# Kernel tuning notes

Hardware: AMD Instinct MI355X
Metric: run time of the kernel (lower is better)

## Reference

```python
import jax, jax.numpy as jnp
import numpy as np

N_NODES = 50000
N_EDGES = 600000
DIM = 128


def setup_inputs() -> dict:
    key = jax.random.key(0)
    k1, k2, k3 = jax.random.split(key, 3)
    x = jax.random.normal(k1, (N_NODES, DIM), dtype=jnp.float32)
    edge_index = jax.random.randint(k2, (2, N_EDGES), 0, N_NODES, dtype=jnp.int64)
    # Xavier-uniform linear weight, torch layout [out_dim, in_dim]
    limit = float(np.sqrt(6.0 / (DIM + DIM)))
    W = jax.random.uniform(k3, (DIM, DIM), dtype=jnp.float32, minval=-limit, maxval=limit)
    return {"x": x, "edge_index": edge_index, "N": N_NODES, "W": W}


def reference(x, edge_index, N, W):
    src, dst = edge_index[0], edge_index[1]
    # in-degree via scatter-add of ones
    deg = jnp.zeros((N,), dtype=x.dtype).at[dst].add(1.0)
    deg_inv_sqrt = jax.lax.rsqrt(deg + 1.0)  # (deg + 1)^-0.5
    h = x * deg_inv_sqrt[:, None]                      # [N, D]
    # gather source features, scatter-add into destinations
    agg = jnp.zeros((N, x.shape[-1]), dtype=x.dtype).at[dst].add(h[src])
    agg = (agg + x) * deg_inv_sqrt[:, None]
    # Linear (no bias, torch weight layout) + ReLU
    return jax.nn.relu(agg @ W.T)
```

## Files before the change

kernel.cpp:

```cpp
#include <hip/hip_runtime.h>

#define DIM 128
#define CAP 48

typedef __attribute__((ext_vector_type(8))) short short8;
typedef __attribute__((ext_vector_type(4))) float floatx4;

__device__ inline unsigned bf16pack2(float a, float b) {
    unsigned ua = __float_as_uint(a), ub = __float_as_uint(b);
    ua = (ua + 0x7fffu + ((ua >> 16) & 1u)) >> 16;
    ub = (ub + 0x7fffu + ((ub >> 16) & 1u)) >> 16;
    return ua | (ub << 16);
}
__device__ inline float bflo(unsigned u) { return __uint_as_float(u << 16); }
__device__ inline float bfhi(unsigned u) { return __uint_as_float(u & 0xffff0000u); }

__global__ __launch_bounds__(256) void prep_kernel(int* __restrict__ degi, int nclr4,
                                                   int clearBlocks,
                                                   const float4* __restrict__ W4,
                                                   uint4* __restrict__ wbf,
                                                   const int* __restrict__ ei, int E,
                                                   int* __restrict__ flag) {
    int b = blockIdx.x;
    if (b < clearBlocks) {
        int i = b * 256 + threadIdx.x;
        if (i < nclr4) ((uint4*)degi)[i] = (uint4){0u, 0u, 0u, 0u};
    } else if (b < clearBlocks + 8) {
        int gw = (b - clearBlocks) * 256 + threadIdx.x;
        if (gw < 2048) {
            float4 lo = W4[(size_t)gw * 2];
            float4 hi = W4[(size_t)gw * 2 + 1];
            uint4 o;
            o.x = bf16pack2(lo.x, lo.y);
            o.y = bf16pack2(lo.z, lo.w);
            o.z = bf16pack2(hi.x, hi.y);
            o.w = bf16pack2(hi.z, hi.w);
            wbf[gw] = o;
        }
    } else {
        __shared__ int nz;
        if (threadIdx.x == 0) nz = 0;
        __syncthreads();
        int found = 0;
        for (int i = threadIdx.x; i < 2048; i += 256)
            if (i < E && ei[2 * i + 1] != 0) found = 1;
        if (found) atomicOr(&nz, 1);
        __syncthreads();
        if (threadIdx.x == 0) *flag = (nz == 0) ? 1 : 0;
    }
}

__global__ __launch_bounds__(256) void insert_kernel(const int* __restrict__ ei, int E,
                                                     unsigned M8,
                                                     const int* __restrict__ flag,
                                                     int* __restrict__ degi,
                                                     int* __restrict__ ssrc) {
    int is64 = *flag;
    unsigned cls = blockIdx.x & 7;
    int tstride4 = (gridDim.x >> 3) * 256 * 4;
    int t0 = ((blockIdx.x >> 3) * 256 + threadIdx.x) * 4;

    for (int e0 = t0; e0 < E; e0 += tstride4) {
        int s[4], d[4];
        if (is64) {
            const int* sw = ei + (size_t)2 * e0;
            int4 a0 = *(const int4*)sw;
            int4 a1 = *(const int4*)(sw + 4);
            s[0] = a0.x; s[1] = a0.z; s[2] = a1.x; s[3] = a1.z;
            const int* dw = ei + (size_t)2 * E + (size_t)2 * e0;
            int4 q0 = *(const int4*)dw;
            int4 q1 = *(const int4*)(dw + 4);
            d[0] = q0.x; d[1] = q0.z; d[2] = q1.x; d[3] = q1.z;
        } else {
            int4 a = *(const int4*)(ei + e0);
            s[0] = a.x; s[1] = a.y; s[2] = a.z; s[3] = a.w;
            int4 q = *(const int4*)(ei + (size_t)E + e0);
            d[0] = q.x; d[1] = q.y; d[2] = q.z; d[3] = q.w;
        }
#pragma unroll
        for (int k = 0; k < 4; ++k) {
            int e = e0 + k;
            if (e >= E) break;
            unsigned p = (unsigned)(((unsigned long long)(unsigned)d[k] * M8) >> 32);
            if (p != cls) continue;
            int slot = atomicAdd(&degi[d[k]], 1);
            if (slot < CAP)
                ssrc[(size_t)d[k] * CAP + slot] = s[k];
        }
    }
}

__global__ __launch_bounds__(256) void scale_kernel(const float4* __restrict__ x4,
                                                    const int* __restrict__ degi,
                                                    uint4* __restrict__ xh, int N) {
    int g = blockIdx.x * 256 + threadIdx.x;
    if (g >= N * 16) return;
    int n = g >> 4;
    float c = rsqrtf((float)degi[n] + 1.0f);
    float4 lo = x4[(size_t)g * 2];
    float4 hi = x4[(size_t)g * 2 + 1];
    uint4 o;
    o.x = bf16pack2(lo.x * c, lo.y * c);
    o.y = bf16pack2(lo.z * c, lo.w * c);
    o.z = bf16pack2(hi.x * c, hi.y * c);
    o.w = bf16pack2(hi.z * c, hi.w * c);
    xh[g] = o;
}

__global__ __launch_bounds__(256) void gather_kernel(const int* __restrict__ degi,
                                                     const int* __restrict__ ssrc,
                                                     const uint4* __restrict__ xh,
                                                     uint4* __restrict__ t, int N) {
    int g = threadIdx.x >> 4;
    int lane = threadIdx.x & 15;
    int n = blockIdx.x * 16 + g;
    if (n >= N) return;
    int deg = degi[n];
    int cnt = deg < CAP ? deg : CAP;
    const int* seg = ssrc + (size_t)n * CAP;

    uint4 self = xh[(size_t)n * 16 + lane];
    float acc[8] = {0.f, 0.f, 0.f, 0.f, 0.f, 0.f, 0.f, 0.f};

#define ADD8(v)                                            \
    {                                                      \
        acc[0] += bflo(v.x); acc[1] += bfhi(v.x);          \
        acc[2] += bflo(v.y); acc[3] += bfhi(v.y);          \
        acc[4] += bflo(v.z); acc[5] += bfhi(v.z);          \
        acc[6] += bflo(v.w); acc[7] += bfhi(v.w);          \
    }

    int j = 0;
    for (; j + 7 < cnt; j += 8) {
        int s0 = seg[j], s1 = seg[j + 1], s2 = seg[j + 2], s3 = seg[j + 3];
        int s4 = seg[j + 4], s5 = seg[j + 5], s6 = seg[j + 6], s7 = seg[j + 7];
        uint4 v0 = xh[(size_t)s0 * 16 + lane];
        uint4 v1 = xh[(size_t)s1 * 16 + lane];
        uint4 v2 = xh[(size_t)s2 * 16 + lane];
        uint4 v3 = xh[(size_t)s3 * 16 + lane];
        uint4 v4 = xh[(size_t)s4 * 16 + lane];
        uint4 v5 = xh[(size_t)s5 * 16 + lane];
        uint4 v6 = xh[(size_t)s6 * 16 + lane];
        uint4 v7 = xh[(size_t)s7 * 16 + lane];
        ADD8(v0); ADD8(v1); ADD8(v2); ADD8(v3);
        ADD8(v4); ADD8(v5); ADD8(v6); ADD8(v7);
    }
    if (j + 3 < cnt) {
        int s0 = seg[j], s1 = seg[j + 1], s2 = seg[j + 2], s3 = seg[j + 3];
        uint4 v0 = xh[(size_t)s0 * 16 + lane];
        uint4 v1 = xh[(size_t)s1 * 16 + lane];
        uint4 v2 = xh[(size_t)s2 * 16 + lane];
        uint4 v3 = xh[(size_t)s3 * 16 + lane];
        ADD8(v0); ADD8(v1); ADD8(v2); ADD8(v3);
        j += 4;
    }
    for (; j < cnt; ++j) {
        uint4 v = xh[(size_t)seg[j] * 16 + lane];
        ADD8(v);
    }
#undef ADD8

    float dn = rsqrtf((float)deg + 1.0f);
    uint4 o;
    o.x = bf16pack2(bflo(self.x) + acc[0] * dn, bfhi(self.x) + acc[1] * dn);
    o.y = bf16pack2(bflo(self.y) + acc[2] * dn, bfhi(self.y) + acc[3] * dn);
    o.z = bf16pack2(bflo(self.z) + acc[4] * dn, bfhi(self.z) + acc[5] * dn);
    o.w = bf16pack2(bflo(self.w) + acc[6] * dn, bfhi(self.w) + acc[7] * dn);
    t[(size_t)n * 16 + lane] = o;
}

__global__ __launch_bounds__(256) void gemm_relu_kernel(const char* __restrict__ t,
                                                        const char* __restrict__ wbf,
                                                        float* __restrict__ out, int N) {
    int tid = threadIdx.x;
    int w = tid >> 6, l = tid & 63;
    int q = l >> 4, m = l & 15;
    int wrow0 = blockIdx.x * 128 + w * 32;

    short8 a[2][4];
#pragma unroll
    for (int rf = 0; rf < 2; ++rf) {
        int r = wrow0 + rf * 16 + m;
        if (r > N - 1) r = N - 1;
        const char* rb = t + (size_t)r * 256 + q * 16;
#pragma unroll
        for (int c = 0; c < 4; ++c)
            a[rf][c] = *(const short8*)(rb + 64 * c);
    }

    floatx4 acc[2][8];
#pragma unroll
    for (int rf = 0; rf < 2; ++rf)
#pragma unroll
        for (int cf = 0; cf < 8; ++cf)
            acc[rf][cf] = (floatx4){0.f, 0.f, 0.f, 0.f};

#pragma unroll
    for (int c = 0; c < 4; ++c) {
#pragma unroll
        for (int cf = 0; cf < 8; ++cf) {
            short8 b = *(const short8*)(wbf + (size_t)(cf * 16 + m) * 256 + q * 16 + 64 * c);
            acc[0][cf] = __builtin_amdgcn_mfma_f32_16x16x32_bf16(a[0][c], b, acc[0][cf], 0, 0, 0);
            acc[1][cf] = __builtin_amdgcn_mfma_f32_16x16x32_bf16(a[1][c], b, acc[1][cf], 0, 0, 0);
        }
    }

#pragma unroll
    for (int rf = 0; rf < 2; ++rf)
#pragma unroll
        for (int j = 0; j < 4; ++j) {
            int r = wrow0 + rf * 16 + q * 4 + j;
            if (r < N) {
#pragma unroll
                for (int cf = 0; cf < 8; ++cf)
                    out[(size_t)r * 128 + cf * 16 + m] = fmaxf(acc[rf][cf][j], 0.0f);
            }
        }
}

extern "C" void kernel_launch(void* const* d_in, const int* in_sizes, int n_in,
                              void* d_out, int out_size, void* d_ws, size_t ws_size,
                              hipStream_t stream) {
    const float* x = (const float*)d_in[0];
    const int* ei = (const int*)d_in[1];
    const float* W = (const float*)d_in[3];
    float* out = (float*)d_out;

    int N = in_sizes[0] / DIM;
    int E = in_sizes[1] / 2;
    unsigned M8 = (unsigned)(((unsigned long long)8 << 32) / (unsigned)N);

    auto align256 = [](size_t v) { return (v + 255) & ~(size_t)255; };
    char* ws = (char*)d_ws;
    size_t off = 0;
    int* degi = (int*)(ws + off);   off += align256((size_t)N * 4);
    int* ssrc = (int*)(ws + off);   off += align256((size_t)N * CAP * 4);
    char* xh = ws + off;            off += align256((size_t)N * 256);
    char* t = ws + off;             off += align256((size_t)N * 256);
    char* wbf = ws + off;           off += align256((size_t)32 * 1024);
    int* flag = (int*)(ws + off);   off += 256;

    int nclr4 = (N + 3) / 4;
    int clearBlocks = (nclr4 + 255) / 256;
    prep_kernel<<<clearBlocks + 9, 256, 0, stream>>>(degi, nclr4, clearBlocks,
                                                     (const float4*)W, (uint4*)wbf,
                                                     ei, E, flag);
    insert_kernel<<<2048, 256, 0, stream>>>(ei, E, M8, flag, degi, ssrc);
    scale_kernel<<<(N * 16 + 255) / 256, 256, 0, stream>>>((const float4*)x, degi,
                                                           (uint4*)xh, N);
    gather_kernel<<<(N + 15) / 16, 256, 0, stream>>>(degi, ssrc, (const uint4*)xh,
                                                     (uint4*)t, N);
    gemm_relu_kernel<<<(N + 127) / 128, 256, 0, stream>>>(t, wbf, out, N);
}
```

Baseline: 85.47 us.

## Replace global-atomic edge insertion with two-pass class partition and LDS bucketing

The single insert kernel, which did global atomics on per-node degree counters, is replaced by a pack kernel and a bucket kernel. The pack kernel partitions edges into 8 destination-range classes using LDS counters and one global cursor atomic per class per block, storing packed 16-bit src/dst pairs. The bucket kernel then has each block scan its class buffer and fill a 256-node range using LDS atomics, writing degrees directly, so the degree-clear pass is no longer needed. This relies on node ids fitting in 16 bits and on each class holding at most CAPC edges. Every bucket block rescans its whole class buffer, which adds read traffic in exchange for fewer global atomics.

```diff
diff --git a/kernel.cpp b/kernel.cpp
--- a/kernel.cpp
+++ b/kernel.cpp
@@ -2,6 +2,10 @@
 
 #define DIM 128
 #define CAP 48
+#define NCLS 8
+#define CLS_SHIFT 13
+#define GRPS 32
+#define CAPC 131072
 
 typedef __attribute__((ext_vector_type(8))) short short8;
 typedef __attribute__((ext_vector_type(4))) float floatx4;
@@ -15,18 +19,14 @@
 __device__ inline float bflo(unsigned u) { return __uint_as_float(u << 16); }
 __device__ inline float bfhi(unsigned u) { return __uint_as_float(u & 0xffff0000u); }
 
-__global__ __launch_bounds__(256) void prep_kernel(int* __restrict__ degi, int nclr4,
-                                                   int clearBlocks,
-                                                   const float4* __restrict__ W4,
+__global__ __launch_bounds__(256) void prep_kernel(const float4* __restrict__ W4,
                                                    uint4* __restrict__ wbf,
                                                    const int* __restrict__ ei, int E,
-                                                   int* __restrict__ flag) {
+                                                   int* __restrict__ flag,
+                                                   int* __restrict__ cursor) {
     int b = blockIdx.x;
-    if (b < clearBlocks) {
-        int i = b * 256 + threadIdx.x;
-        if (i < nclr4) ((uint4*)degi)[i] = (uint4){0u, 0u, 0u, 0u};
-    } else if (b < clearBlocks + 8) {
-        int gw = (b - clearBlocks) * 256 + threadIdx.x;
+    if (b < 8) {
+        int gw = b * 256 + threadIdx.x;
         if (gw < 2048) {
             float4 lo = W4[(size_t)gw * 2];
             float4 hi = W4[(size_t)gw * 2 + 1];
@@ -38,6 +38,7 @@
             wbf[gw] = o;
         }
     } else {
+        if (threadIdx.x < NCLS) cursor[threadIdx.x] = 0;
         __shared__ int nz;
         if (threadIdx.x == 0) nz = 0;
         __syncthreads();
@@ -50,18 +51,19 @@
     }
 }
 
-__global__ __launch_bounds__(256) void insert_kernel(const int* __restrict__ ei, int E,
-                                                     unsigned M8,
-                                                     const int* __restrict__ flag,
-                                                     int* __restrict__ degi,
-                                                     int* __restrict__ ssrc) {
+__global__ __launch_bounds__(512) void pack_kernel(const int* __restrict__ ei, int E,
+                                                   const int* __restrict__ flag,
+                                                   int* __restrict__ cursor,
+                                                   unsigned* __restrict__ classbuf) {
+    __shared__ int lcnt[NCLS], lbase[NCLS];
+    if (threadIdx.x < NCLS) lcnt[threadIdx.x] = 0;
+    __syncthreads();
+
     int is64 = *flag;
-    unsigned cls = blockIdx.x & 7;
-    int tstride4 = (gridDim.x >> 3) * 256 * 4;
-    int t0 = ((blockIdx.x >> 3) * 256 + threadIdx.x) * 4;
-
-    for (int e0 = t0; e0 < E; e0 += tstride4) {
-        int s[4], d[4];
+    int e0 = (blockIdx.x * 512 + threadIdx.x) * 4;
+    int s[4], d[4], r[4], c[4];
+    bool act = (e0 < E);
+    if (act) {
         if (is64) {
             const int* sw = ei + (size_t)2 * e0;
             int4 a0 = *(const int4*)sw;
@@ -79,15 +81,66 @@
         }
 #pragma unroll
         for (int k = 0; k < 4; ++k) {
-            int e = e0 + k;
-            if (e >= E) break;
-            unsigned p = (unsigned)(((unsigned long long)(unsigned)d[k] * M8) >> 32);
-            if (p != cls) continue;
-            int slot = atomicAdd(&degi[d[k]], 1);
-            if (slot < CAP)
-                ssrc[(size_t)d[k] * CAP + slot] = s[k];
-        }
-    }
+            if (e0 + k < E) {
+                c[k] = d[k] >> CLS_SHIFT;
+                r[k] = atomicAdd(&lcnt[c[k]], 1);
+            } else c[k] = -1;
+        }
+    } else {
+#pragma unroll
+        for (int k = 0; k < 4; ++k) c[k] = -1;
+    }
+    __syncthreads();
+    if (threadIdx.x < NCLS && lcnt[threadIdx.x] > 0)
+        lbase[threadIdx.x] = atomicAdd(&cursor[threadIdx.x], lcnt[threadIdx.x]);
+    __syncthreads();
+#pragma unroll
+    for (int k = 0; k < 4; ++k) {
+        if (c[k] >= 0) {
+            int idx = lbase[c[k]] + r[k];
+            if (idx < CAPC)
+                classbuf[(size_t)c[k] * CAPC + idx] =
+                    ((unsigned)s[k] << 16) | (unsigned)d[k];
+        }
+    }
+}
+
+__global__ __launch_bounds__(256) void bucket_kernel(const unsigned* __restrict__ classbuf,
+                                                     const int* __restrict__ cursor,
+                                                     int* __restrict__ degi,
+                                                     int* __restrict__ ssrc, int N) {
+    int c = blockIdx.x >> 5, g = blockIdx.x & (GRPS - 1);
+    int lo = (c << CLS_SHIFT) + (g << 8);
+    int hi = lo + 256 < N ? lo + 256 : N;
+    __shared__ int cnt[256];
+    cnt[threadIdx.x] = 0;
+    __syncthreads();
+
+    if (lo < N) {
+        int len = cursor[c];
+        if (len > CAPC) len = CAPC;
+        const unsigned* buf = classbuf + (size_t)c * CAPC;
+
+#define PROC(u)                                                        \
+        {                                                              \
+            int dd = (int)((u) & 0xffffu);                             \
+            if (dd >= lo && dd < hi) {                                 \
+                int slot = atomicAdd(&cnt[dd - lo], 1);                \
+                if (slot < CAP)                                        \
+                    ssrc[(size_t)dd * CAP + slot] = (int)((u) >> 16);  \
+            }                                                          \
+        }
+        int nvec = len >> 2;
+        for (int i = threadIdx.x; i < nvec; i += 256) {
+            uint4 p = ((const uint4*)buf)[i];
+            PROC(p.x); PROC(p.y); PROC(p.z); PROC(p.w);
+        }
+        for (int i = (nvec << 2) + threadIdx.x; i < len; i += 256) PROC(buf[i]);
+#undef PROC
+    }
+    __syncthreads();
+    int n = lo + threadIdx.x;
+    if (n < hi) degi[n] = cnt[threadIdx.x];
 }
 
 __global__ __launch_bounds__(256) void scale_kernel(const float4* __restrict__ x4,
@@ -228,24 +281,23 @@
 
     int N = in_sizes[0] / DIM;
     int E = in_sizes[1] / 2;
-    unsigned M8 = (unsigned)(((unsigned long long)8 << 32) / (unsigned)N);
 
     auto align256 = [](size_t v) { return (v + 255) & ~(size_t)255; };
     char* ws = (char*)d_ws;
     size_t off = 0;
-    int* degi = (int*)(ws + off);   off += align256((size_t)N * 4);
-    int* ssrc = (int*)(ws + off);   off += align256((size_t)N * CAP * 4);
-    char* xh = ws + off;            off += align256((size_t)N * 256);
-    char* t = ws + off;             off += align256((size_t)N * 256);
-    char* wbf = ws + off;           off += align256((size_t)32 * 1024);
-    int* flag = (int*)(ws + off);   off += 256;
-
-    int nclr4 = (N + 3) / 4;
-    int clearBlocks = (nclr4 + 255) / 256;
-    prep_kernel<<<clearBlocks + 9, 256, 0, stream>>>(degi, nclr4, clearBlocks,
-                                                     (const float4*)W, (uint4*)wbf,
-                                                     ei, E, flag);
-    insert_kernel<<<2048, 256, 0, stream>>>(ei, E, M8, flag, degi, ssrc);
+    int* degi = (int*)(ws + off);      off += align256((size_t)N * 4);
+    int* ssrc = (int*)(ws + off);      off += align256((size_t)N * CAP * 4);
+    char* xh = ws + off;               off += align256((size_t)N * 256);
+    char* t = ws + off;                off += align256((size_t)N * 256);
+    char* wbf = ws + off;              off += align256((size_t)32 * 1024);
+    int* flag = (int*)(ws + off);      off += 256;
+    int* cursor = (int*)(ws + off);    off += 256;
+    unsigned* classbuf = (unsigned*)(ws + off);
+    off += align256((size_t)NCLS * CAPC * 4);
+
+    prep_kernel<<<9, 256, 0, stream>>>((const float4*)W, (uint4*)wbf, ei, E, flag, cursor);
+    pack_kernel<<<(E / 4 + 511) / 512, 512, 0, stream>>>(ei, E, flag, cursor, classbuf);
+    bucket_kernel<<<NCLS * GRPS, 256, 0, stream>>>(classbuf, cursor, degi, ssrc, N);
     scale_kernel<<<(N * 16 + 255) / 256, 256, 0, stream>>>((const float4*)x, degi,
                                                            (uint4*)xh, N);
     gather_kernel<<<(N + 15) / 16, 256, 0, stream>>>(degi, ssrc, (const uint4*)xh,
```

Result: slower. 117.9 us (+38.0%).
